# Optimization experiments

Measured on AMD Instinct MI355X. Metric: run time of the kernel, lower is better.

## Reference

```python
import jax, jax.numpy as jnp
from jax import lax
import numpy as np

LRELU_SLOPE = 0.2
DEMOD_EPS = 1e-8


def _mod_conv(x, style, weight, bias, demodulate, pad):
    """StyleGAN2 modulated conv via grouped conv (groups = batch).
    x: [B,Cin,H,W]; style: [B,Cin]; weight: [Cout,Cin,kh,kw]; bias: [Cout]."""
    B, Cin, H, W = x.shape
    Cout, _, kh, kw = weight.shape
    # per-sample modulated weight [B,Cout,Cin,kh,kw]
    wt = weight[None] * style[:, None, :, None, None]
    if demodulate:
        wt = wt / jnp.sqrt(jnp.sum(wt ** 2, axis=(2, 3, 4), keepdims=True) + DEMOD_EPS)
    out = lax.conv_general_dilated(
        x.reshape(1, B * Cin, H, W),
        wt.reshape(B * Cout, Cin, kh, kw),
        window_strides=(1, 1),
        padding=[(pad, pad), (pad, pad)],
        dimension_numbers=('NCHW', 'OIHW', 'NCHW'),
        feature_group_count=B,
    )
    return out.reshape(B, Cout, H, W) + bias[None, :, None, None]


def setup_inputs() -> dict:
    key = jax.random.key(0)
    ks = jax.random.split(key, 16)
    B, Cin, Cout, Wd, H = 4, 512, 256, 512, 64
    f32 = jnp.float32
    d = {
        'x': jax.random.normal(ks[0], (B, Cin, H, H), f32),
        'w': jax.random.normal(ks[1], (B, Wd), f32),
        # conv1: Cin->Cout 3x3
        'w1': jax.random.normal(ks[2], (Cout, Cin, 3, 3), f32) / np.float32(np.sqrt(Cin * 9)),
        'b1': jax.random.normal(ks[3], (Cout,), f32) * 0.01,
        'a1w': jax.random.normal(ks[4], (Cin, Wd), f32) / np.float32(np.sqrt(Wd)),
        'a1b': jnp.ones((Cin,), f32),
        # conv2: Cout->Cout 3x3
        'w2': jax.random.normal(ks[5], (Cout, Cout, 3, 3), f32) / np.float32(np.sqrt(Cout * 9)),
        'b2': jax.random.normal(ks[6], (Cout,), f32) * 0.01,
        'a2w': jax.random.normal(ks[7], (Cout, Wd), f32) / np.float32(np.sqrt(Wd)),
        'a2b': jnp.ones((Cout,), f32),
        # to_rgb: Cout->3 1x1, no demodulation
        'w3': jax.random.normal(ks[8], (3, Cout, 1, 1), f32) / np.float32(np.sqrt(Cout)),
        'b3': jax.random.normal(ks[9], (3,), f32) * 0.01,
        'a3w': jax.random.normal(ks[10], (Cout, Wd), f32) / np.float32(np.sqrt(Wd)),
        'a3b': jnp.ones((Cout,), f32),
    }
    return d


def reference(x, w, w1, b1, a1w, a1b, w2, b2, a2w, a2b, w3, b3, a3w, a3b):
    B, C, H, W = x.shape
    # nn.Upsample(scale_factor=2, mode='bilinear', align_corners=False) == half-pixel bilinear
    xu = jax.image.resize(x, (B, C, 2 * H, 2 * W), method='bilinear')
    s1 = w @ a1w.T + a1b                      # affine -> per-sample style [B,Cin]
    h = jax.nn.leaky_relu(_mod_conv(xu, s1, w1, b1, True, 1), LRELU_SLOPE)
    s2 = w @ a2w.T + a2b
    h = jax.nn.leaky_relu(_mod_conv(h, s2, w2, b2, True, 1), LRELU_SLOPE)
    s3 = w @ a3w.T + a3b
    rgb = jax.nn.leaky_relu(_mod_conv(h, s3, w3, b3, False, 0), LRELU_SLOPE)
    return (h, rgb)
```

## Files before the change

### kernel.cpp

```cpp
#include <hip/hip_runtime.h>
#include <stdint.h>

typedef __attribute__((ext_vector_type(8))) short bhalf8;
typedef __attribute__((ext_vector_type(4))) float fx4;

__device__ __forceinline__ unsigned short f2bf(float f) {
    unsigned u = __builtin_bit_cast(unsigned, f);
    unsigned r = (u + 0x7fffu + ((u >> 16) & 1u)) >> 16;
    return (unsigned short)r;
}
__device__ __forceinline__ float bf2f(unsigned short h) {
    unsigned u = ((unsigned)h) << 16;
    return __builtin_bit_cast(float, u);
}
__device__ __forceinline__ float lrelu(float v) { return v > 0.f ? v : 0.2f * v; }

typedef __attribute__((address_space(1))) void as1_void;
typedef __attribute__((address_space(3))) void as3_void;
__device__ __forceinline__ void gl_lds16(const void* g, void* l) {
    __builtin_amdgcn_global_load_lds((as1_void*)(void*)g, (as3_void*)l, 16, 0, 0);
}

__global__ __launch_bounds__(256) void style_kernel(
    const float* __restrict__ w,
    const float* __restrict__ a1w, const float* __restrict__ a1b,
    const float* __restrict__ a2w, const float* __restrict__ a2b,
    const float* __restrict__ a3w, const float* __restrict__ a3b,
    float* __restrict__ s1, float* __restrict__ s2, float* __restrict__ s3)
{
    int gw = blockIdx.x * 4 + (threadIdx.x >> 6);
    int lane = threadIdx.x & 63;
    int b = gw >> 10, r = gw & 1023;
    const float* arow; const float* abias; float* dst;
    if (r < 512)      { arow = a1w + (size_t)r * 512;        abias = a1b + r;       dst = s1 + b * 512 + r; }
    else if (r < 768) { int rr = r - 512; arow = a2w + (size_t)rr * 512; abias = a2b + rr; dst = s2 + b * 256 + rr; }
    else              { int rr = r - 768; arow = a3w + (size_t)rr * 512; abias = a3b + rr; dst = s3 + b * 256 + rr; }
    const float* wrow = w + b * 512;
    float acc = 0.f;
    #pragma unroll
    for (int j = 0; j < 8; ++j) {
        int c = lane + j * 64;
        acc += wrow[c] * arow[c];
    }
    #pragma unroll
    for (int off = 32; off; off >>= 1) acc += __shfl_down(acc, off, 64);
    if (lane == 0) *dst = acc + *abias;
}

__global__ __launch_bounds__(256) void demod_kernel(
    const float* __restrict__ w1, const float* __restrict__ w2,
    const float* __restrict__ s1, const float* __restrict__ s2,
    float* __restrict__ d1, float* __restrict__ d2)
{
    int blk = blockIdx.x;
    int conv = blk >> 10, b = (blk >> 8) & 3, o = blk & 255;
    int t = threadIdx.x;
    int cin = conv ? 256 : 512;
    const float* s = conv ? (s2 + b * 256) : (s1 + b * 512);
    const float* row = (conv ? w2 : w1) + (size_t)o * cin * 9;
    __shared__ float sv[512];
    for (int i = t; i < cin; i += 256) { float v = s[i]; sv[i] = v * v; }
    __syncthreads();
    float sum = 0.f;
    int n = cin * 9;
    for (int k = t; k < n; k += 256) {
        float v = row[k];
        sum += v * v * sv[k / 9];
    }
    #pragma unroll
    for (int off = 32; off; off >>= 1) sum += __shfl_down(sum, off, 64);
    __shared__ float red[4];
    if ((t & 63) == 0) red[t >> 6] = sum;
    __syncthreads();
    if (t == 0) {
        float tot = red[0] + red[1] + red[2] + red[3];
        (conv ? d2 : d1)[b * 256 + o] = rsqrtf(tot + 1e-8f);
    }
}

__global__ __launch_bounds__(256) void pack_kernel(
    const float* __restrict__ w1, const float* __restrict__ w2,
    unsigned short* __restrict__ wp1, unsigned short* __restrict__ wp2)
{
    int tid = blockIdx.x * 256 + threadIdx.x;
    const int N1 = 1179648, N2 = 589824;
    if (tid < N1) {
        int e = tid & 7, m = (tid >> 3) & 127, kh = (tid >> 10) & 3;
        int dx = (tid >> 12) % 3, ic = (tid / 12288) & 15;
        int dy = (tid / 196608) % 3, mblk = tid / 589824;
        int o = mblk * 128 + m, ci = ic * 32 + kh * 8 + e;
        wp1[tid] = f2bf(w1[((size_t)o * 512 + ci) * 9 + dy * 3 + dx]);
    } else if (tid < N1 + N2) {
        int t2 = tid - N1;
        int e = t2 & 7, m = (t2 >> 3) & 127, kh = (t2 >> 10) & 3;
        int dx = (t2 >> 12) % 3, ic = (t2 / 12288) & 7;
        int dy = (t2 / 98304) % 3, mblk = t2 / 294912;
        int o = mblk * 128 + m, ci = ic * 32 + kh * 8 + e;
        wp2[t2] = f2bf(w2[((size_t)o * 256 + ci) * 9 + dy * 3 + dx]);
    }
}

__global__ __launch_bounds__(256) void upsample_kernel(
    const float* __restrict__ x, const float* __restrict__ s1,
    unsigned short* __restrict__ xu)
{
    __shared__ float L[2][64][65];
    int bid = blockIdx.x, t = threadIdx.x;
    int yo = bid & 127, b = bid >> 7;
    int k = yo >> 1;
    int sy0, sy1; float wy0, wy1;
    if ((yo & 1) == 0) { sy0 = k > 0 ? k - 1 : 0; sy1 = k; wy0 = 0.25f; wy1 = 0.75f; }
    else               { sy0 = k; sy1 = k < 63 ? k + 1 : 63; wy0 = 0.75f; wy1 = 0.25f; }
    for (int c0 = 0; c0 < 512; c0 += 64) {
        __syncthreads();
        #pragma unroll
        for (int j = 0; j < 32; ++j) {
            int f = t + j * 256;
            int idx = f & 63, rowid = f >> 6;
            int cc = rowid & 63, which = rowid >> 6;
            int sy = which ? sy1 : sy0;
            L[which][cc][idx] = x[((size_t)(b * 512 + c0 + cc) * 64 + sy) * 64 + idx];
        }
        __syncthreads();
        #pragma unroll
        for (int j = 0; j < 16; ++j) {
            int it = t + j * 256;
            int cp = it & 31, xo = it >> 5;
            int kk = xo >> 1, sx0, sx1; float wx0, wx1;
            if ((xo & 1) == 0) { sx0 = kk > 0 ? kk - 1 : 0; sx1 = kk; wx0 = 0.25f; wx1 = 0.75f; }
            else               { sx0 = kk; sx1 = kk < 63 ? kk + 1 : 63; wx0 = 0.75f; wx1 = 0.25f; }
            int c = cp * 2;
            float A0 = wx0 * L[0][c][sx0] + wx1 * L[0][c][sx1];
            float B0 = wx0 * L[1][c][sx0] + wx1 * L[1][c][sx1];
            float A1 = wx0 * L[0][c + 1][sx0] + wx1 * L[0][c + 1][sx1];
            float B1 = wx0 * L[1][c + 1][sx0] + wx1 * L[1][c + 1][sx1];
            float v0 = (wy0 * A0 + wy1 * B0) * s1[b * 512 + c0 + c];
            float v1 = (wy0 * A1 + wy1 * B1) * s1[b * 512 + c0 + c + 1];
            unsigned pk = (unsigned)f2bf(v0) | ((unsigned)f2bf(v1) << 16);
            *(unsigned*)&xu[((size_t)(b * 128 + yo) * 128 + xo) * 512 + c0 + c] = pk;
        }
    }
}

template<int CIN, bool IS_CONV2>
__global__ __launch_bounds__(512, 4) void conv3x3_kernel(
    const unsigned short* __restrict__ inp,
    const unsigned short* __restrict__ wpack,
    const float* __restrict__ dvec,
    const float* __restrict__ bias,
    const float* __restrict__ post,
    unsigned short* __restrict__ outmod,
    float* __restrict__ outf)
{
    constexpr int NIC = CIN / 32;
    __shared__ __attribute__((aligned(16))) short Blds[2][4][4160];
    const int tid = threadIdx.x;
    const int lane = tid & 63;
    const int wvi = tid >> 6;
    const int bid = blockIdx.x;
    const int y0 = (bid & 63) << 1;
    const int mblk = (bid >> 6) & 1;
    const int b = bid >> 7;
    const int wm = (wvi >> 2) * 64;
    const int row = (wvi >> 1) & 1;
    const int wn = (wvi & 1) * 64;
    const int lhi = lane >> 4;
    const int llo = lane & 15;

    if (tid < 64) {
        int buf = tid >> 5, rr = (tid >> 3) & 3, slot = ((tid >> 2) & 1) ? 129 : 0, part = tid & 3;
        *(int4*)((char*)&Blds[buf][rr][0] + slot * 64 + part * 16) = make_int4(0, 0, 0, 0);
    }

    const int xg = tid >> 2, i8 = tid & 3;
    const int i8s = i8 ^ ((xg >> 1) & 3);

    fx4 acc[4][4];
    #pragma unroll
    for (int mt = 0; mt < 4; ++mt)
        #pragma unroll
        for (int nt = 0; nt < 4; ++nt) acc[mt][nt] = (fx4){0.f, 0.f, 0.f, 0.f};

    auto stageB = [&](int buf, int ic) {
        #pragma unroll
        for (int rr = 0; rr < 4; ++rr) {
            const int yy = y0 - 1 + rr;
            char* dstB = (char*)&Blds[buf][rr][0] + 64 + tid * 16;
            if ((unsigned)yy < 128u) {
                gl_lds16(inp + ((size_t)(b * 128 + yy) * 128 + xg) * CIN + ic * 32 + i8s * 8, dstB);
            } else {
                *(int4*)dstB = make_int4(0, 0, 0, 0);
            }
        }
    };

    stageB(0, 0);
    __syncthreads();

    for (int ic = 0; ic < NIC; ++ic) {
        const int buf = ic & 1;
        if (ic + 1 < NIC) stageB(buf ^ 1, ic + 1);

        #pragma unroll
        for (int dy = 0; dy < 3; ++dy) {
            const short* Brow = &Blds[buf][row + dy][0];
            const unsigned short* abase = wpack + ((size_t)(mblk * 3 + dy) * NIC + ic) * 12288;
            #pragma unroll
            for (int dx = 0; dx < 3; ++dx) {
                bhalf8 af[4], bfr[4];
                #pragma unroll
                for (int mt = 0; mt < 4; ++mt)
                    af[mt] = *(const bhalf8*)(abase + (size_t)dx * 4096
                                              + ((size_t)(lhi * 128 + wm + mt * 16 + llo)) * 8);
                #pragma unroll
                for (int nt = 0; nt < 4; ++nt) {
                    int s = wn + nt * 16 + llo + dx;
                    int key = ((s - 1) >> 1) & 3;
                    bfr[nt] = *(const bhalf8*)&Brow[s * 32 + ((lhi ^ key) << 3)];
                }
                __builtin_amdgcn_s_setprio(1);
                #pragma unroll
                for (int mt = 0; mt < 4; ++mt)
                    #pragma unroll
                    for (int nt = 0; nt < 4; ++nt)
                        acc[mt][nt] = __builtin_amdgcn_mfma_f32_16x16x32_bf16(
                            af[mt], bfr[nt], acc[mt][nt], 0, 0, 0);
                __builtin_amdgcn_s_setprio(0);
            }
        }
        __syncthreads();
    }

    const int y = y0 + row;
    #pragma unroll
    for (int mt = 0; mt < 4; ++mt) {
        const int o0 = mblk * 128 + wm + mt * 16 + lhi * 4;
        const fx4 d4 = *(const fx4*)(dvec + b * 256 + o0);
        const fx4 bb4 = *(const fx4*)(bias + o0);
        const fx4 p4 = *(const fx4*)(post + b * 256 + o0);
        #pragma unroll
        for (int nt = 0; nt < 4; ++nt) {
            const int xo = wn + nt * 16 + llo;
            unsigned lo = 0, hi = 0;
            #pragma unroll
            for (int r = 0; r < 4; ++r) {
                float v = acc[mt][nt][r] * d4[r] + bb4[r];
                v = lrelu(v);
                if (IS_CONV2)
                    outf[(((size_t)b * 256 + o0 + r) * 128 + y) * 128 + xo] = v;
                unsigned short ub = f2bf(v * p4[r]);
                if (r < 2) lo |= (unsigned)ub << (16 * r);
                else       hi |= (unsigned)ub << (16 * (r - 2));
            }
            *(uint2*)&outmod[((size_t)(b * 128 + y) * 128 + xo) * 256 + o0] = make_uint2(lo, hi);
        }
    }
}

__global__ __launch_bounds__(256) void rgb_kernel(
    const unsigned short* __restrict__ hs3,
    const float* __restrict__ w3, const float* __restrict__ b3,
    float* __restrict__ out)
{
    __shared__ float wl[768];
    int t = threadIdx.x;
    for (int i = t; i < 768; i += 256) wl[i] = w3[i];
    __syncthreads();
    int p = blockIdx.x * 64 + (t >> 2);
    int q = t & 3;
    const unsigned short* src = hs3 + (size_t)p * 256 + q * 64;
    float a0 = 0.f, a1 = 0.f, a2 = 0.f;
    #pragma unroll
    for (int c8 = 0; c8 < 64; c8 += 8) {
        int4 pk = *(const int4*)(src + c8);
        #pragma unroll
        for (int qq = 0; qq < 4; ++qq) {
            unsigned uu = ((const unsigned*)&pk)[qq];
            float ve = bf2f((unsigned short)(uu & 0xffffu));
            float vo = bf2f((unsigned short)(uu >> 16));
            int c = q * 64 + c8 + qq * 2;
            a0 += ve * wl[c] + vo * wl[c + 1];
            a1 += ve * wl[256 + c] + vo * wl[256 + c + 1];
            a2 += ve * wl[512 + c] + vo * wl[512 + c + 1];
        }
    }
    a0 += __shfl_xor(a0, 1, 64); a0 += __shfl_xor(a0, 2, 64);
    a1 += __shfl_xor(a1, 1, 64); a1 += __shfl_xor(a1, 2, 64);
    a2 += __shfl_xor(a2, 1, 64); a2 += __shfl_xor(a2, 2, 64);
    int b = p >> 14, yx = p & 16383;
    if (q < 3) {
        float v = (q == 0) ? a0 : (q == 1) ? a1 : a2;
        out[((size_t)b * 3 + q) * 16384 + yx] = lrelu(v + b3[q]);
    }
}

extern "C" void kernel_launch(void* const* d_in, const int* in_sizes, int n_in,
                              void* d_out, int out_size, void* d_ws, size_t ws_size,
                              hipStream_t stream) {
    const float* x   = (const float*)d_in[0];
    const float* w   = (const float*)d_in[1];
    const float* w1  = (const float*)d_in[2];
    const float* b1  = (const float*)d_in[3];
    const float* a1w = (const float*)d_in[4];
    const float* a1b = (const float*)d_in[5];
    const float* w2  = (const float*)d_in[6];
    const float* b2  = (const float*)d_in[7];
    const float* a2w = (const float*)d_in[8];
    const float* a2b = (const float*)d_in[9];
    const float* w3  = (const float*)d_in[10];
    const float* b3  = (const float*)d_in[11];
    const float* a3w = (const float*)d_in[12];
    const float* a3b = (const float*)d_in[13];

    char* ws = (char*)d_ws;
    unsigned short* xu  = (unsigned short*)(ws);
    unsigned short* hs3 = (unsigned short*)(ws);
    unsigned short* t1  = (unsigned short*)(ws + 67108864);
    unsigned short* wp1 = (unsigned short*)(ws + 100663296);
    unsigned short* wp2 = (unsigned short*)(ws + 103022592);
    float* s1 = (float*)(ws + 104202240);
    float* s2 = (float*)(ws + 104210432);
    float* s3 = (float*)(ws + 104214528);
    float* d1 = (float*)(ws + 104218624);
    float* d2 = (float*)(ws + 104222720);

    float* h_out   = (float*)d_out;
    float* rgb_out = h_out + 16777216;

    style_kernel<<<1024, 256, 0, stream>>>(w, a1w, a1b, a2w, a2b, a3w, a3b, s1, s2, s3);
    demod_kernel<<<2048, 256, 0, stream>>>(w1, w2, s1, s2, d1, d2);
    pack_kernel<<<6912, 256, 0, stream>>>(w1, w2, wp1, wp2);
    upsample_kernel<<<512, 256, 0, stream>>>(x, s1, xu);
    conv3x3_kernel<512, false><<<512, 512, 0, stream>>>(xu, wp1, d1, b1, s2, t1, nullptr);
    conv3x3_kernel<256, true><<<512, 512, 0, stream>>>(t1, wp2, d2, b2, s3, hs3, h_out);
    rgb_kernel<<<1024, 256, 0, stream>>>(hs3, w3, b3, rgb_out);
}
```

Measured before the change: 400.6 us.

## Stage conv weights through LDS double buffer, single-buffer input rows

The conv3x3 kernel now copies each (ic,dy) weight slab into a double-buffered LDS tile using global_load_lds, so A fragments are read from LDS instead of directly from global memory. The input-row buffer becomes single-buffered without zero-padding slots, and the edge columns are zeroed in registers with a select. This is meant to cut redundant global and L2 traffic for weights, which are shared across the eight waves. In exchange it adds a barrier per dy step, and the next input stage is no longer overlapped with compute.

```diff
diff --git a/kernel.cpp b/kernel.cpp
--- a/kernel.cpp
+++ b/kernel.cpp
@@ -153,7 +153,8 @@
     float* __restrict__ outf)
 {
     constexpr int NIC = CIN / 32;
-    __shared__ __attribute__((aligned(16))) short Blds[2][4][4160];
+    __shared__ __attribute__((aligned(16))) short Alds[2][12288];
+    __shared__ __attribute__((aligned(16))) short Blds[4][128][32];
     const int tid = threadIdx.x;
     const int lane = tid & 63;
     const int wvi = tid >> 6;
@@ -167,11 +168,6 @@
     const int lhi = lane >> 4;
     const int llo = lane & 15;
 
-    if (tid < 64) {
-        int buf = tid >> 5, rr = (tid >> 3) & 3, slot = ((tid >> 2) & 1) ? 129 : 0, part = tid & 3;
-        *(int4*)((char*)&Blds[buf][rr][0] + slot * 64 + part * 16) = make_int4(0, 0, 0, 0);
-    }
-
     const int xg = tid >> 2, i8 = tid & 3;
     const int i8s = i8 ^ ((xg >> 1) & 3);
 
@@ -181,11 +177,11 @@
         #pragma unroll
         for (int nt = 0; nt < 4; ++nt) acc[mt][nt] = (fx4){0.f, 0.f, 0.f, 0.f};
 
-    auto stageB = [&](int buf, int ic) {
+    auto stageB = [&](int ic) {
         #pragma unroll
         for (int rr = 0; rr < 4; ++rr) {
             const int yy = y0 - 1 + rr;
-            char* dstB = (char*)&Blds[buf][rr][0] + 64 + tid * 16;
+            char* dstB = (char*)&Blds[rr][0][0] + tid * 16;
             if ((unsigned)yy < 128u) {
                 gl_lds16(inp + ((size_t)(b * 128 + yy) * 128 + xg) * CIN + ic * 32 + i8s * 8, dstB);
             } else {
@@ -193,30 +189,52 @@
             }
         }
     };
-
-    stageB(0, 0);
+    auto stageA = [&](int ic, int dy, int buf) {
+        const unsigned short* asrc = wpack + ((size_t)(mblk * 3 + dy) * NIC + ic) * 12288;
+        #pragma unroll
+        for (int j = 0; j < 3; ++j) {
+            int g = tid + j * 512;
+            gl_lds16(asrc + (size_t)g * 8, (char*)&Alds[buf][0] + g * 16);
+        }
+    };
+
+    stageB(0);
+    stageA(0, 0, 0);
     __syncthreads();
 
+    int par = 0;
     for (int ic = 0; ic < NIC; ++ic) {
-        const int buf = ic & 1;
-        if (ic + 1 < NIC) stageB(buf ^ 1, ic + 1);
-
         #pragma unroll
         for (int dy = 0; dy < 3; ++dy) {
-            const short* Brow = &Blds[buf][row + dy][0];
-            const unsigned short* abase = wpack + ((size_t)(mblk * 3 + dy) * NIC + ic) * 12288;
+            const bool last = (ic == NIC - 1) && (dy == 2);
+            if (!last) {
+                const int nic = (dy == 2) ? ic + 1 : ic;
+                const int ndy = (dy == 2) ? 0 : dy + 1;
+                stageA(nic, ndy, par ^ 1);
+            }
+            const short* Ab = &Alds[par][0];
+            const short* Brow = &Blds[row + dy][0][0];
             #pragma unroll
             for (int dx = 0; dx < 3; ++dx) {
                 bhalf8 af[4], bfr[4];
                 #pragma unroll
                 for (int mt = 0; mt < 4; ++mt)
-                    af[mt] = *(const bhalf8*)(abase + (size_t)dx * 4096
-                                              + ((size_t)(lhi * 128 + wm + mt * 16 + llo)) * 8);
+                    af[mt] = *(const bhalf8*)&Ab[dx * 4096 + (lhi * 128 + wm + mt * 16 + llo) * 8];
                 #pragma unroll
                 for (int nt = 0; nt < 4; ++nt) {
-                    int s = wn + nt * 16 + llo + dx;
-                    int key = ((s - 1) >> 1) & 3;
-                    bfr[nt] = *(const bhalf8*)&Brow[s * 32 + ((lhi ^ key) << 3)];
+                    const int s = wn + nt * 16 + llo + dx;
+                    if ((nt == 0 && dx == 0) || (nt == 3 && dx == 2)) {
+                        const bool edge = (s == 0) || (s == 129);
+                        const int sp = edge ? 0 : (s - 1);
+                        const int key = (sp >> 1) & 3;
+                        bhalf8 v = *(const bhalf8*)&Brow[sp * 32 + ((lhi ^ key) << 3)];
+                        bhalf8 z = {0, 0, 0, 0, 0, 0, 0, 0};
+                        bfr[nt] = edge ? z : v;
+                    } else {
+                        const int sp = s - 1;
+                        const int key = (sp >> 1) & 3;
+                        bfr[nt] = *(const bhalf8*)&Brow[sp * 32 + ((lhi ^ key) << 3)];
+                    }
                 }
                 __builtin_amdgcn_s_setprio(1);
                 #pragma unroll
@@ -227,8 +245,13 @@
                             af[mt], bfr[nt], acc[mt][nt], 0, 0, 0);
                 __builtin_amdgcn_s_setprio(0);
             }
-        }
-        __syncthreads();
+            if (dy == 2 && ic + 1 < NIC) {
+                __syncthreads();
+                stageB(ic + 1);
+            }
+            if (!last) __syncthreads();
+            par ^= 1;
+        }
     }
 
     const int y = y0 + row;
```

Result: faster. 370.4 us (-7.5%).

## Stage conv weight tiles into LDS with async triple-buffered pipeline

Applied to the files above, without the earlier changes.

Weight (A) fragments were previously read directly from global memory by each wave. They are now loaded into a triple-buffered LDS region through global_load_lds, one buffer per dy tap. Hand-placed vmcnt waits and bare s_barrier calls replace __syncthreads so that A and B staging overlap with MFMA work. The larger LDS footprint lowers the launch-bounds occupancy hint from 4 to 2, and the manual vmcnt counting depends on the exact number of loads issued, including the halo-row case.

```diff
diff --git a/kernel.cpp b/kernel.cpp
--- a/kernel.cpp
+++ b/kernel.cpp
@@ -143,7 +143,7 @@
 }
 
 template<int CIN, bool IS_CONV2>
-__global__ __launch_bounds__(512, 4) void conv3x3_kernel(
+__global__ __launch_bounds__(512, 2) void conv3x3_kernel(
     const unsigned short* __restrict__ inp,
     const unsigned short* __restrict__ wpack,
     const float* __restrict__ dvec,
@@ -153,6 +153,7 @@
     float* __restrict__ outf)
 {
     constexpr int NIC = CIN / 32;
+    __shared__ __attribute__((aligned(16))) short Alds[3][12288];
     __shared__ __attribute__((aligned(16))) short Blds[2][4][4160];
     const int tid = threadIdx.x;
     const int lane = tid & 63;
@@ -166,6 +167,7 @@
     const int wn = (wvi & 1) * 64;
     const int lhi = lane >> 4;
     const int llo = lane & 15;
+    const int halo = (y0 == 0 || y0 == 126) ? 1 : 0;
 
     if (tid < 64) {
         int buf = tid >> 5, rr = (tid >> 3) & 3, slot = ((tid >> 2) & 1) ? 129 : 0, part = tid & 3;
@@ -193,29 +195,56 @@
             }
         }
     };
-
+    auto stageA = [&](int ic, int dy, int buf) {
+        const unsigned short* asrc = wpack + ((size_t)(mblk * 3 + dy) * NIC + ic) * 12288;
+        #pragma unroll
+        for (int j = 0; j < 3; ++j) {
+            int g = tid + j * 512;
+            gl_lds16(asrc + (size_t)g * 8, (char*)&Alds[buf][0] + g * 16);
+        }
+    };
+
+    stageA(0, 0, 0);
+    asm volatile("" ::: "memory");
     stageB(0, 0);
-    __syncthreads();
+    asm volatile("" ::: "memory");
+    stageA(0, 1, 1);
 
     for (int ic = 0; ic < NIC; ++ic) {
-        const int buf = ic & 1;
-        if (ic + 1 < NIC) stageB(buf ^ 1, ic + 1);
-
         #pragma unroll
         for (int dy = 0; dy < 3; ++dy) {
-            const short* Brow = &Blds[buf][row + dy][0];
-            const unsigned short* abase = wpack + ((size_t)(mblk * 3 + dy) * NIC + ic) * 12288;
+            if (dy == 0) {
+                asm volatile("s_waitcnt vmcnt(3) lgkmcnt(0)" ::: "memory");
+            } else if (ic == NIC - 1) {
+                if (dy == 1) { asm volatile("s_waitcnt vmcnt(3) lgkmcnt(0)" ::: "memory"); }
+                else         { asm volatile("s_waitcnt vmcnt(0) lgkmcnt(0)" ::: "memory"); }
+            } else if (halo) {
+                asm volatile("s_waitcnt vmcnt(6) lgkmcnt(0)" ::: "memory");
+            } else {
+                asm volatile("s_waitcnt vmcnt(7) lgkmcnt(0)" ::: "memory");
+            }
+            __builtin_amdgcn_s_barrier();
+            if (dy == 0) {
+                stageA(ic, 2, 2);
+                asm volatile("" ::: "memory");
+                if (ic + 1 < NIC) stageB((ic + 1) & 1, ic + 1);
+            } else if (dy == 1) {
+                if (ic + 1 < NIC) stageA(ic + 1, 0, 0);
+            } else {
+                if (ic + 1 < NIC) stageA(ic + 1, 1, 1);
+            }
+            const short* Ab = &Alds[dy][0];
+            const short* Brow = &Blds[ic & 1][row + dy][0];
             #pragma unroll
             for (int dx = 0; dx < 3; ++dx) {
                 bhalf8 af[4], bfr[4];
                 #pragma unroll
                 for (int mt = 0; mt < 4; ++mt)
-                    af[mt] = *(const bhalf8*)(abase + (size_t)dx * 4096
-                                              + ((size_t)(lhi * 128 + wm + mt * 16 + llo)) * 8);
+                    af[mt] = *(const bhalf8*)&Ab[dx * 4096 + (lhi * 128 + wm + mt * 16 + llo) * 8];
                 #pragma unroll
                 for (int nt = 0; nt < 4; ++nt) {
-                    int s = wn + nt * 16 + llo + dx;
-                    int key = ((s - 1) >> 1) & 3;
+                    const int s = wn + nt * 16 + llo + dx;
+                    const int key = ((s - 1) >> 1) & 3;
                     bfr[nt] = *(const bhalf8*)&Brow[s * 32 + ((lhi ^ key) << 3)];
                 }
                 __builtin_amdgcn_s_setprio(1);
@@ -228,7 +257,6 @@
                 __builtin_amdgcn_s_setprio(0);
             }
         }
-        __syncthreads();
     }
 
     const int y = y0 + row;
```

Result: slower. 415.1 us (+3.6%).
